# Performance work log

Measured on AMD Instinct MI355X. Metric: run time of the kernel, lower is better.

The kernel has to match this reference:

```python
import jax, jax.numpy as jnp
from jax import lax
import numpy as np

B, T, D, K = 64, 512, 768, 32


def setup_inputs() -> dict:
    key = jax.random.key(0)
    ks = jax.random.split(key, 6)
    x = jax.random.normal(ks[0], (B, T, D), dtype=jnp.float32)
    labels = jax.random.randint(ks[1], (B, T), 0, K)
    mask = jnp.ones((B, T), dtype=bool)  # mask[:,0] must be True for torchcrf
    W = jax.random.normal(ks[2], (D, K), dtype=jnp.float32) * (1.0 / np.sqrt(D))
    b = jnp.zeros((K,), dtype=jnp.float32)
    # CRF params (torchcrf init: uniform(-0.1, 0.1))
    start_trans = jax.random.uniform(ks[3], (K,), minval=-0.1, maxval=0.1, dtype=jnp.float32)
    end_trans = jax.random.uniform(ks[4], (K,), minval=-0.1, maxval=0.1, dtype=jnp.float32)
    trans = jax.random.uniform(ks[5], (K, K), minval=-0.1, maxval=0.1, dtype=jnp.float32)
    return {"x": x, "labels": labels, "mask": mask, "W": W, "b": b,
            "start_trans": start_trans, "end_trans": end_trans, "trans": trans}


def reference(x, labels, mask, W, b, start_trans, end_trans, trans):
    emissions = jnp.einsum('btd,dk->btk', x, W) + b  # [B,T,K]
    Bn, Tn, Kn = emissions.shape
    maskf = mask.astype(emissions.dtype)

    # ---- numerator: score of the gold tag path ----
    first_tags = labels[:, 0]
    num = start_trans[first_tags] + emissions[jnp.arange(Bn), 0, first_tags]
    prev, cur = labels[:, :-1], labels[:, 1:]
    em_gold = jnp.take_along_axis(emissions[:, 1:], cur[..., None], axis=-1)[..., 0]  # [B,T-1]
    num = num + jnp.sum((trans[prev, cur] + em_gold) * maskf[:, 1:], axis=1)
    seq_len = jnp.sum(mask.astype(jnp.int32), axis=1)  # [B]
    last_tags = jnp.take_along_axis(labels, (seq_len - 1)[:, None], axis=1)[:, 0]
    num = num + end_trans[last_tags]

    # ---- denominator: forward-algorithm log partition via scan ----
    def step(score, inp):
        em_t, m_t = inp  # em_t: [B,K], m_t: [B] bool
        # score[b,i] + trans[i,j] + em_t[b,j] -> logsumexp over i
        nxt = jax.nn.logsumexp(score[:, :, None] + trans[None, :, :] + em_t[:, None, :], axis=1)
        return jnp.where(m_t[:, None], nxt, score), None

    init = start_trans[None, :] + emissions[:, 0]  # [B,K]
    em_rest = jnp.swapaxes(emissions[:, 1:], 0, 1)  # [T-1,B,K]
    m_rest = jnp.swapaxes(mask[:, 1:], 0, 1)        # [T-1,B]
    score, _ = lax.scan(step, init, (em_rest, m_rest))
    denom = jax.nn.logsumexp(score + end_trans[None, :], axis=-1)  # [B]

    llh = num - denom
    return -jnp.mean(llh)  # module returns -crf(..., reduction='mean')
```

## Files before the change

### kernel.cpp

```cpp
#include <hip/hip_runtime.h>


#define BB 64
#define TT 512
#define DD 768
#define KK 32
#define INV_LN2 1.44269504088896f
#define LN2f    0.69314718055994f

typedef __attribute__((ext_vector_type(8))) short bf16x8;
typedef __attribute__((ext_vector_type(8))) _Float16 f16x8;
typedef __attribute__((ext_vector_type(4))) float f32x4;
typedef __attribute__((ext_vector_type(16))) float f32x16;

__device__ __forceinline__ float fexp2(float x) { float r; asm("v_exp_f32 %0, %1" : "=v"(r) : "v"(x)); return r; }
__device__ __forceinline__ float flog2(float x) { float r; asm("v_log_f32 %0, %1" : "=v"(r) : "v"(x)); return r; }

__device__ __forceinline__ bf16x8 cvt8(float4 a, float4 b) {
    union { int i[4]; bf16x8 v; } u;
    asm("v_cvt_pk_bf16_f32 %0, %1, %2" : "=v"(u.i[0]) : "v"(a.x), "v"(a.y));
    asm("v_cvt_pk_bf16_f32 %0, %1, %2" : "=v"(u.i[1]) : "v"(a.z), "v"(a.w));
    asm("v_cvt_pk_bf16_f32 %0, %1, %2" : "=v"(u.i[2]) : "v"(b.x), "v"(b.y));
    asm("v_cvt_pk_bf16_f32 %0, %1, %2" : "=v"(u.i[3]) : "v"(b.z), "v"(b.w));
    return u.v;
}
__device__ __forceinline__ bf16x8 asbf(float4 b) {
    union { float4 f; bf16x8 v; } u; u.f = b; return u.v;
}
__device__ __forceinline__ f16x8 frag4h(int a, int b, int c, int d) {
    union { int i[4]; f16x8 v; } u; u.i[0] = a; u.i[1] = b; u.i[2] = c; u.i[3] = d; return u.v;
}
__device__ __forceinline__ void plswap(int& a, int& b) {
    asm("v_permlane32_swap_b32 %0, %1" : "+v"(a), "+v"(b));
}
__device__ __forceinline__ int pkmulh(int a, int b) {
    int r; asm("v_pk_mul_f16 %0, %1, %2" : "=v"(r) : "v"(a), "v"(b)); return r;
}
__device__ __forceinline__ int cvtrep(float e) {
    int r; asm("v_cvt_pkrtz_f16_f32 %0, %1, %1" : "=v"(r) : "v"(e)); return r;
}
__device__ __forceinline__ int cvtpkh(float a, float b) {
    int r; asm("v_cvt_pkrtz_f16_f32 %0, %1, %2" : "=v"(r) : "v"(a), "v"(b)); return r;
}

__global__ __launch_bounds__(256) void pack_w(const float* __restrict__ W, float4* __restrict__ Wb)
{
    int idx = blockIdx.x * 256 + threadIdx.x;
    int l = idx & 63, slice = idx >> 6;
    int ks = slice >> 1, t = slice & 1;
    int c = (l & 15) + t * 16, g = l >> 4;
    int kr = ks * 32 + g * 8;
    float f0 = W[(kr + 0) * KK + c], f1 = W[(kr + 1) * KK + c];
    float f2 = W[(kr + 2) * KK + c], f3 = W[(kr + 3) * KK + c];
    float f4 = W[(kr + 4) * KK + c], f5 = W[(kr + 5) * KK + c];
    float f6 = W[(kr + 6) * KK + c], f7 = W[(kr + 7) * KK + c];
    union { int i[4]; float4 f; } u;
    asm("v_cvt_pk_bf16_f32 %0, %1, %2" : "=v"(u.i[0]) : "v"(f0), "v"(f1));
    asm("v_cvt_pk_bf16_f32 %0, %1, %2" : "=v"(u.i[1]) : "v"(f2), "v"(f3));
    asm("v_cvt_pk_bf16_f32 %0, %1, %2" : "=v"(u.i[2]) : "v"(f4), "v"(f5));
    asm("v_cvt_pk_bf16_f32 %0, %1, %2" : "=v"(u.i[3]) : "v"(f6), "v"(f7));
    Wb[idx] = u.f;
}

__global__ __launch_bounds__(256) void emis_kernel(
    const float* __restrict__ x, const float4* __restrict__ Wb,
    const float* __restrict__ bias, float* __restrict__ emlin)
{
    const int tid = threadIdx.x;
    const int l = tid & 63, wave = tid >> 6;
    const int r = l & 15, g = l >> 4;
    const int row0 = (blockIdx.x * 4 + wave) * 16;

    const float4* xA = (const float4*)x + (size_t)(row0 + r) * 192 + g * 2;
    const float4* wb = Wb + l;

    f32x4 acc0 = {0.f, 0.f, 0.f, 0.f};
    f32x4 acc1 = {0.f, 0.f, 0.f, 0.f};

    float4 s0a0, s0a1, s0b0, s0b1;
    float4 s1a0, s1a1, s1b0, s1b1;
    float4 s2a0, s2a1, s2b0, s2b1;
    float4 s3a0, s3a1, s3b0, s3b1;

#define LOADS(P, ks_) \
    P##a0 = xA[(ks_) * 8]; P##a1 = xA[(ks_) * 8 + 1]; \
    P##b0 = wb[(ks_) * 128]; P##b1 = wb[(ks_) * 128 + 64];
#define CONS(P) { \
    bf16x8 av = cvt8(P##a0, P##a1); \
    acc0 = __builtin_amdgcn_mfma_f32_16x16x32_bf16(av, asbf(P##b0), acc0, 0, 0, 0); \
    acc1 = __builtin_amdgcn_mfma_f32_16x16x32_bf16(av, asbf(P##b1), acc1, 0, 0, 0); }

    LOADS(s0, 0) LOADS(s1, 1) LOADS(s2, 2) LOADS(s3, 3)
    for (int ks = 0; ks < 20; ks += 4) {
        CONS(s0) LOADS(s0, ks + 4)
        CONS(s1) LOADS(s1, ks + 5)
        CONS(s2) LOADS(s2, ks + 6)
        CONS(s3) LOADS(s3, ks + 7)
    }
    CONS(s0) CONS(s1) CONS(s2) CONS(s3)
#undef LOADS
#undef CONS

    const int c0 = l & 15;
    const float b0 = bias[c0], b1 = bias[c0 + 16];
    #pragma unroll
    for (int reg = 0; reg < 4; ++reg) {
        const int orow = row0 + g * 4 + reg;
        emlin[(size_t)orow * KK + c0]      = fexp2((acc0[reg] + b0) * INV_LN2);
        emlin[(size_t)orow * KK + c0 + 16] = fexp2((acc1[reg] + b1) * INV_LN2);
    }
}

__global__ __launch_bounds__(64) void chain_kernel(
    const float* __restrict__ emlin, const float* __restrict__ trans,
    float* __restrict__ Qg, int* __restrict__ eag)
{
    __shared__ float els[34 * KK];

    const int g = blockIdx.x;
    const int b = g >> 4, u = g & 15;
    const int l = threadIdx.x;
    const int r32 = l & 31, hf = l >> 5;
    const float* el_g = emlin + (size_t)b * TT * KK;
    const int t0 = 32 * u + 1;

    #pragma unroll
    for (int i = 0; i < 17; ++i) {
        int idx = i * 64 + l;
        int gidx = t0 * KK + idx;
        if (gidx > TT * KK - 1) gidx = TT * KK - 1;
        els[idx] = el_g[gidx];
    }

    int M1p0, M1p1, M1p2, M1p3, M2p0, M2p1, M2p2, M2p3;
    {
        float m[16];
        #pragma unroll
        for (int e = 0; e < 8; ++e) {
            m[e]     = fexp2(trans[(hf * 8 + e) * KK + r32] * INV_LN2);
            m[e + 8] = fexp2(trans[(16 + hf * 8 + e) * KK + r32] * INV_LN2);
        }
        M1p0 = cvtpkh(m[0], m[1]);   M1p1 = cvtpkh(m[2], m[3]);
        M1p2 = cvtpkh(m[4], m[5]);   M1p3 = cvtpkh(m[6], m[7]);
        M2p0 = cvtpkh(m[8], m[9]);   M2p1 = cvtpkh(m[10], m[11]);
        M2p2 = cvtpkh(m[12], m[13]); M2p3 = cvtpkh(m[14], m[15]);
    }
    __syncthreads();

    int Ba0, Ba1, Ba2, Ba3, Ba4, Ba5, Ba6, Ba7;
    int Bb0, Bb1, Bb2, Bb3, Bb4, Bb5, Bb6, Bb7;
    {
        #define IDP(kl) (((r32 == (kl)) ? 0x3C00 : 0) | ((r32 == (kl) + 1) ? 0x3C000000 : 0))
        int k0 = hf * 8;
        Ba0 = IDP(k0);      Ba1 = IDP(k0 + 2);  Ba2 = IDP(k0 + 4);  Ba3 = IDP(k0 + 6);
        Ba4 = IDP(k0 + 16); Ba5 = IDP(k0 + 18); Ba6 = IDP(k0 + 20); Ba7 = IDP(k0 + 22);
        Bb0 = Ba0; Bb1 = Ba1; Bb2 = Ba2; Bb3 = Ba3;
        Bb4 = Ba4; Bb5 = Ba5; Bb6 = Ba6; Bb7 = Ba7;
        #undef IDP
    }
    const f32x16 zf = {0,0,0,0, 0,0,0,0, 0,0,0,0, 0,0,0,0};
    f32x16 acca = zf, accb = zf;
    int EEa = 0, EEb = 0;
    int eaca_ = 0, eacb_ = 0;

    float eva = els[r32];
    float evb = els[16 * KK + r32];

#define CLAMP14(E) ((E) < -14 ? -14 : ((E) > 14 ? 14 : (E)))

#define STEP1(X, rnext) { \
    int Ec = CLAMP14(EE##X); \
    eac##X##_ += Ec; \
    int scb = (15 - Ec) << 10; scb |= (scb << 16); \
    int ep = pkmulh(cvtrep(ev##X), scb); \
    ev##X = els[(rnext) * KK + r32]; \
    int A0 = pkmulh(M1p0, ep), A1 = pkmulh(M1p1, ep), A2 = pkmulh(M1p2, ep), A3 = pkmulh(M1p3, ep); \
    int A4 = pkmulh(M2p0, ep), A5 = pkmulh(M2p1, ep), A6 = pkmulh(M2p2, ep), A7 = pkmulh(M2p3, ep); \
    acc##X = __builtin_amdgcn_mfma_f32_32x32x16_f16(frag4h(A0, A1, A2, A3), \
                 frag4h(B##X##0, B##X##1, B##X##2, B##X##3), zf, 0, 0, 0); \
    acc##X = __builtin_amdgcn_mfma_f32_32x32x16_f16(frag4h(A4, A5, A6, A7), \
                 frag4h(B##X##4, B##X##5, B##X##6, B##X##7), acc##X, 0, 0, 0); \
    EE##X = (int)((((unsigned)__builtin_amdgcn_readfirstlane(__float_as_int(acc##X[0]))) >> 23) & 0xFFu) - 127; \
    int u0 = cvtpkh(acc##X[0],  acc##X[1]),  u1 = cvtpkh(acc##X[2],  acc##X[3]); \
    int u2 = cvtpkh(acc##X[4],  acc##X[5]),  u3 = cvtpkh(acc##X[6],  acc##X[7]); \
    int u4 = cvtpkh(acc##X[8],  acc##X[9]),  u5 = cvtpkh(acc##X[10], acc##X[11]); \
    int u6 = cvtpkh(acc##X[12], acc##X[13]), u7 = cvtpkh(acc##X[14], acc##X[15]); \
    plswap(u0, u2); plswap(u1, u3); plswap(u4, u6); plswap(u5, u7); \
    B##X##0 = u0; B##X##1 = u1; B##X##2 = u2; B##X##3 = u3; \
    B##X##4 = u4; B##X##5 = u5; B##X##6 = u6; B##X##7 = u7; \
}

#define STEP2(rna, rnb) { \
    int EcA = CLAMP14(EEa), EcB = CLAMP14(EEb); \
    eaca_ += EcA; eacb_ += EcB; \
    int scbA = (15 - EcA) << 10; scbA |= (scbA << 16); \
    int scbB = (15 - EcB) << 10; scbB |= (scbB << 16); \
    int epA = pkmulh(cvtrep(eva), scbA); \
    int epB = pkmulh(cvtrep(evb), scbB); \
    eva = els[(rna) * KK + r32]; \
    evb = els[(rnb) * KK + r32]; \
    int Aa0 = pkmulh(M1p0, epA), Aa1 = pkmulh(M1p1, epA), Aa2 = pkmulh(M1p2, epA), Aa3 = pkmulh(M1p3, epA); \
    int Ab0 = pkmulh(M1p0, epB), Ab1 = pkmulh(M1p1, epB), Ab2 = pkmulh(M1p2, epB), Ab3 = pkmulh(M1p3, epB); \
    int Aa4 = pkmulh(M2p0, epA), Aa5 = pkmulh(M2p1, epA), Aa6 = pkmulh(M2p2, epA), Aa7 = pkmulh(M2p3, epA); \
    int Ab4 = pkmulh(M2p0, epB), Ab5 = pkmulh(M2p1, epB), Ab6 = pkmulh(M2p2, epB), Ab7 = pkmulh(M2p3, epB); \
    acca = __builtin_amdgcn_mfma_f32_32x32x16_f16(frag4h(Aa0, Aa1, Aa2, Aa3), \
               frag4h(Ba0, Ba1, Ba2, Ba3), zf, 0, 0, 0); \
    accb = __builtin_amdgcn_mfma_f32_32x32x16_f16(frag4h(Ab0, Ab1, Ab2, Ab3), \
               frag4h(Bb0, Bb1, Bb2, Bb3), zf, 0, 0, 0); \
    acca = __builtin_amdgcn_mfma_f32_32x32x16_f16(frag4h(Aa4, Aa5, Aa6, Aa7), \
               frag4h(Ba4, Ba5, Ba6, Ba7), acca, 0, 0, 0); \
    accb = __builtin_amdgcn_mfma_f32_32x32x16_f16(frag4h(Ab4, Ab5, Ab6, Ab7), \
               frag4h(Bb4, Bb5, Bb6, Bb7), accb, 0, 0, 0); \
    EEa = (int)((((unsigned)__builtin_amdgcn_readfirstlane(__float_as_int(acca[0]))) >> 23) & 0xFFu) - 127; \
    int ua0 = cvtpkh(acca[0],  acca[1]),  ua1 = cvtpkh(acca[2],  acca[3]); \
    int ua2 = cvtpkh(acca[4],  acca[5]),  ua3 = cvtpkh(acca[6],  acca[7]); \
    int ua4 = cvtpkh(acca[8],  acca[9]),  ua5 = cvtpkh(acca[10], acca[11]); \
    int ua6 = cvtpkh(acca[12], acca[13]), ua7 = cvtpkh(acca[14], acca[15]); \
    EEb = (int)((((unsigned)__builtin_amdgcn_readfirstlane(__float_as_int(accb[0]))) >> 23) & 0xFFu) - 127; \
    int ub0 = cvtpkh(accb[0],  accb[1]),  ub1 = cvtpkh(accb[2],  accb[3]); \
    int ub2 = cvtpkh(accb[4],  accb[5]),  ub3 = cvtpkh(accb[6],  accb[7]); \
    int ub4 = cvtpkh(accb[8],  accb[9]),  ub5 = cvtpkh(accb[10], accb[11]); \
    int ub6 = cvtpkh(accb[12], accb[13]), ub7 = cvtpkh(accb[14], accb[15]); \
    plswap(ua0, ua2); plswap(ua1, ua3); plswap(ua4, ua6); plswap(ua5, ua7); \
    plswap(ub0, ub2); plswap(ub1, ub3); plswap(ub4, ub6); plswap(ub5, ub7); \
    Ba0 = ua0; Ba1 = ua1; Ba2 = ua2; Ba3 = ua3; \
    Ba4 = ua4; Ba5 = ua5; Ba6 = ua6; Ba7 = ua7; \
    Bb0 = ub0; Bb1 = ub1; Bb2 = ub2; Bb3 = ub3; \
    Bb4 = ub4; Bb5 = ub5; Bb6 = ub6; Bb7 = ub7; \
}

    #pragma unroll 1
    for (int s = 0; s < 15; ++s) {
        STEP2(s + 1, 17 + s)
    }
    if (u < 15) { STEP2(16, 32) }
    else        { STEP1(a, 16) }
#undef STEP1
#undef STEP2
#undef CLAMP14

    float* Qa = Qg + (size_t)(b * 32 + 2 * u) * 1024;
    float* Qb = Qa + 1024;
    #pragma unroll
    for (int i = 0; i < 16; ++i) {
        int row = (i & 3) + 8 * (i >> 2) + 4 * hf;
        Qa[row * KK + r32] = acca[i];
        Qb[row * KK + r32] = accb[i];
    }
    if (l == 0) { eag[b * 32 + 2 * u] = eaca_; eag[b * 32 + 2 * u + 1] = eacb_; }
}

__global__ __launch_bounds__(64) void combine_kernel(
    const float* __restrict__ emlin, const int* __restrict__ labels,
    const float* __restrict__ start, const float* __restrict__ endt,
    const float* __restrict__ trans, const float* __restrict__ Qg,
    const int* __restrict__ eag, float* __restrict__ llh)
{
    __shared__ float trs[KK * KK];
    __shared__ float wlds[KK];

    const int b = blockIdx.x, l = threadIdx.x;
    const int r32 = l & 31, hf = l >> 5;
    const float* el_g = emlin + (size_t)b * TT * KK;

    for (int i = 0; i < 16; ++i) trs[i * 64 + l] = trans[i * 64 + l];
    __syncthreads();

    const int* lab = labels + b * TT;
    float num = 0.f;
    #pragma unroll
    for (int c = 0; c < 8; ++c) {
        int t = c * 64 + l;
        int cur = lab[t];
        float v = LN2f * flog2(el_g[t * KK + cur]);
        v += (t == 0) ? start[cur] : trs[lab[t - 1] * KK + cur];
        if (t == TT - 1) v += endt[cur];
        num += v;
    }
    #pragma unroll
    for (int o = 32; o; o >>= 1) num += __shfl_xor(num, o);

    if (l < KK) wlds[l] = fexp2(start[l] * INV_LN2) * el_g[l];
    __syncthreads();

    const float4* Qbase = (const float4*)(Qg + (size_t)b * 32 * 1024);
    const int qoff = r32 * 8 + hf * 4;
    const int* eab = eag + b * 32;

    float4 qa0 = Qbase[qoff], qa1 = Qbase[qoff + 1], qa2 = Qbase[qoff + 2], qa3 = Qbase[qoff + 3];
    int Etot = 0;
    float sres = 0.f;
    for (int c = 0; c < 32; ++c) {
        int cn = (c + 1) & 31;
        float4 qb0 = Qbase[cn * 256 + qoff],     qb1 = Qbase[cn * 256 + qoff + 1];
        float4 qb2 = Qbase[cn * 256 + qoff + 2], qb3 = Qbase[cn * 256 + qoff + 3];
        const float4* wv = (const float4*)wlds + hf * 4;
        float4 w0 = wv[0], w1 = wv[1], w2 = wv[2], w3 = wv[3];
        float s = qa0.x * w0.x + qa0.y * w0.y + qa0.z * w0.z + qa0.w * w0.w
                + qa1.x * w1.x + qa1.y * w1.y + qa1.z * w1.z + qa1.w * w1.w
                + qa2.x * w2.x + qa2.y * w2.y + qa2.z * w2.z + qa2.w * w2.w
                + qa3.x * w3.x + qa3.y * w3.y + qa3.z * w3.z + qa3.w * w3.w;
        s += __shfl_xor(s, 32);
        int e0 = (int)((((unsigned)__builtin_amdgcn_readfirstlane(__float_as_int(s))) >> 23) & 0xFFu) - 127;
        if (e0 < -126) e0 = -126;
        if (e0 > 126) e0 = 126;
        Etot += eab[c] + e0;
        sres = s * __int_as_float((127 - e0) << 23);
        __syncthreads();
        if (l < KK) wlds[l] = sres;
        __syncthreads();
        qa0 = qb0; qa1 = qb1; qa2 = qb2; qa3 = qb3;
    }

    float tv = sres * fexp2(endt[r32] * INV_LN2);
    #pragma unroll
    for (int o = 16; o; o >>= 1) tv += __shfl_xor(tv, o);
    float denom = LN2f * ((float)Etot + flog2(tv));
    if (l == 0) llh[b] = num - denom;
}

__global__ __launch_bounds__(64) void reduce_kernel(
    const float* __restrict__ llh, float* __restrict__ out)
{
    const int l = threadIdx.x;
    float v = llh[l];
    #pragma unroll
    for (int o = 32; o; o >>= 1) v += __shfl_xor(v, o);
    if (l == 0) out[0] = -v * (1.0f / BB);
}

extern "C" void kernel_launch(void* const* d_in, const int* in_sizes, int n_in,
                              void* d_out, int out_size, void* d_ws, size_t ws_size,
                              hipStream_t stream)
{
    const float* x      = (const float*)d_in[0];
    const int*   labels = (const int*)  d_in[1];
    const float* W      = (const float*)d_in[3];
    const float* bias   = (const float*)d_in[4];
    const float* start  = (const float*)d_in[5];
    const float* endt   = (const float*)d_in[6];
    const float* trans  = (const float*)d_in[7];
    float* out  = (float*)d_out;

    char* ws = (char*)d_ws;
    float*  emlin = (float*)ws;
    float4* Wb    = (float4*)(ws + (4u << 20));
    float*  Qg    = (float*)(ws + (4u << 20) + (64u << 10));
    int*    eag   = (int*)(ws + (12u << 20) + (64u << 10));
    float*  llh   = (float*)(ws + (12u << 20) + (128u << 10));

    pack_w<<<dim3(12), dim3(256), 0, stream>>>(W, Wb);
    emis_kernel<<<dim3(512), dim3(256), 0, stream>>>(x, Wb, bias, emlin);
    chain_kernel<<<dim3(1024), dim3(64), 0, stream>>>(emlin, trans, Qg, eag);
    combine_kernel<<<dim3(BB), dim3(64), 0, stream>>>(emlin, labels, start, endt, trans, Qg, eag, llh);
    reduce_kernel<<<dim3(1), dim3(64), 0, stream>>>(llh, out);
}
```

Before: 54.87 us.

## Fold weight packing into emission kernel and reduction into combine via atomics

Removes the separate pack_w launch: each emission block now converts W to bf16 into a 48KB shared-memory tile and reads its B operands from LDS. Removes the final reduce launch: combine blocks add fixed-point quantized llh values into a 64-bit atomic, and the last block to finish writes the mean. This cuts two kernel launches and their dependencies, at the cost of every emission block redundantly converting W (extra global reads and a barrier), heavier LDS use per block, and fixed-point rounding in the final sum.

```diff
diff --git a/kernel.cpp b/kernel.cpp
--- a/kernel.cpp
+++ b/kernel.cpp
@@ -43,36 +43,39 @@
     int r; asm("v_cvt_pkrtz_f16_f32 %0, %1, %2" : "=v"(r) : "v"(a), "v"(b)); return r;
 }
 
-__global__ __launch_bounds__(256) void pack_w(const float* __restrict__ W, float4* __restrict__ Wb)
-{
-    int idx = blockIdx.x * 256 + threadIdx.x;
-    int l = idx & 63, slice = idx >> 6;
-    int ks = slice >> 1, t = slice & 1;
-    int c = (l & 15) + t * 16, g = l >> 4;
-    int kr = ks * 32 + g * 8;
-    float f0 = W[(kr + 0) * KK + c], f1 = W[(kr + 1) * KK + c];
-    float f2 = W[(kr + 2) * KK + c], f3 = W[(kr + 3) * KK + c];
-    float f4 = W[(kr + 4) * KK + c], f5 = W[(kr + 5) * KK + c];
-    float f6 = W[(kr + 6) * KK + c], f7 = W[(kr + 7) * KK + c];
-    union { int i[4]; float4 f; } u;
-    asm("v_cvt_pk_bf16_f32 %0, %1, %2" : "=v"(u.i[0]) : "v"(f0), "v"(f1));
-    asm("v_cvt_pk_bf16_f32 %0, %1, %2" : "=v"(u.i[1]) : "v"(f2), "v"(f3));
-    asm("v_cvt_pk_bf16_f32 %0, %1, %2" : "=v"(u.i[2]) : "v"(f4), "v"(f5));
-    asm("v_cvt_pk_bf16_f32 %0, %1, %2" : "=v"(u.i[3]) : "v"(f6), "v"(f7));
-    Wb[idx] = u.f;
-}
-
 __global__ __launch_bounds__(256) void emis_kernel(
-    const float* __restrict__ x, const float4* __restrict__ Wb,
+    const float* __restrict__ x, const float* __restrict__ W,
     const float* __restrict__ bias, float* __restrict__ emlin)
 {
+    __shared__ float4 WbL[3072];
+
     const int tid = threadIdx.x;
+
+    #pragma unroll
+    for (int u0 = 0; u0 < 12; ++u0) {
+        int idx = u0 * 256 + tid;
+        int ll = idx & 63, slice = idx >> 6;
+        int ks = slice >> 1, tt = slice & 1;
+        int c = (ll & 15) + tt * 16, gg = ll >> 4;
+        int kr = ks * 32 + gg * 8;
+        float f0 = W[(kr + 0) * KK + c], f1 = W[(kr + 1) * KK + c];
+        float f2 = W[(kr + 2) * KK + c], f3 = W[(kr + 3) * KK + c];
+        float f4 = W[(kr + 4) * KK + c], f5 = W[(kr + 5) * KK + c];
+        float f6 = W[(kr + 6) * KK + c], f7 = W[(kr + 7) * KK + c];
+        union { int i[4]; float4 f; } u;
+        asm("v_cvt_pk_bf16_f32 %0, %1, %2" : "=v"(u.i[0]) : "v"(f0), "v"(f1));
+        asm("v_cvt_pk_bf16_f32 %0, %1, %2" : "=v"(u.i[1]) : "v"(f2), "v"(f3));
+        asm("v_cvt_pk_bf16_f32 %0, %1, %2" : "=v"(u.i[2]) : "v"(f4), "v"(f5));
+        asm("v_cvt_pk_bf16_f32 %0, %1, %2" : "=v"(u.i[3]) : "v"(f6), "v"(f7));
+        WbL[idx] = u.f;
+    }
+    __syncthreads();
+
     const int l = tid & 63, wave = tid >> 6;
     const int r = l & 15, g = l >> 4;
     const int row0 = (blockIdx.x * 4 + wave) * 16;
 
     const float4* xA = (const float4*)x + (size_t)(row0 + r) * 192 + g * 2;
-    const float4* wb = Wb + l;
 
     f32x4 acc0 = {0.f, 0.f, 0.f, 0.f};
     f32x4 acc1 = {0.f, 0.f, 0.f, 0.f};
@@ -84,7 +87,7 @@
 
 #define LOADS(P, ks_) \
     P##a0 = xA[(ks_) * 8]; P##a1 = xA[(ks_) * 8 + 1]; \
-    P##b0 = wb[(ks_) * 128]; P##b1 = wb[(ks_) * 128 + 64];
+    P##b0 = WbL[(ks_) * 128 + l]; P##b1 = WbL[(ks_) * 128 + 64 + l];
 #define CONS(P) { \
     bf16x8 av = cvt8(P##a0, P##a1); \
     acc0 = __builtin_amdgcn_mfma_f32_16x16x32_bf16(av, asbf(P##b0), acc0, 0, 0, 0); \
@@ -113,7 +116,8 @@
 
 __global__ __launch_bounds__(64) void chain_kernel(
     const float* __restrict__ emlin, const float* __restrict__ trans,
-    float* __restrict__ Qg, int* __restrict__ eag)
+    float* __restrict__ Qg, int* __restrict__ eag,
+    unsigned long long* __restrict__ gsum, unsigned* __restrict__ gcnt)
 {
     __shared__ float els[34 * KK];
 
@@ -123,6 +127,8 @@
     const int r32 = l & 31, hf = l >> 5;
     const float* el_g = emlin + (size_t)b * TT * KK;
     const int t0 = 32 * u + 1;
+
+    if (g == 0 && l == 0) { atomicExch(gsum, 0ull); atomicExch(gcnt, 0u); }
 
     #pragma unroll
     for (int i = 0; i < 17; ++i) {
@@ -254,7 +260,8 @@
     const float* __restrict__ emlin, const int* __restrict__ labels,
     const float* __restrict__ start, const float* __restrict__ endt,
     const float* __restrict__ trans, const float* __restrict__ Qg,
-    const int* __restrict__ eag, float* __restrict__ llh)
+    const int* __restrict__ eag, unsigned long long* __restrict__ gsum,
+    unsigned* __restrict__ gcnt, float* __restrict__ out)
 {
     __shared__ float trs[KK * KK];
     __shared__ float wlds[KK];
@@ -316,17 +323,18 @@
     #pragma unroll
     for (int o = 16; o; o >>= 1) tv += __shfl_xor(tv, o);
     float denom = LN2f * ((float)Etot + flog2(tv));
-    if (l == 0) llh[b] = num - denom;
-}
-
-__global__ __launch_bounds__(64) void reduce_kernel(
-    const float* __restrict__ llh, float* __restrict__ out)
-{
-    const int l = threadIdx.x;
-    float v = llh[l];
-    #pragma unroll
-    for (int o = 32; o; o >>= 1) v += __shfl_xor(v, o);
-    if (l == 0) out[0] = -v * (1.0f / BB);
+    if (l == 0) {
+        float llh = num - denom;
+        long long q = llrintf(llh * 1048576.0f);
+        atomicAdd(gsum, (unsigned long long)q);
+        __threadfence();
+        unsigned done = atomicAdd(gcnt, 1u);
+        if (done == BB - 1) {
+            unsigned long long sfull = atomicAdd(gsum, 0ull);
+            long long ss = (long long)sfull;
+            out[0] = -(float)((double)ss * (1.0 / (1048576.0 * (double)BB)));
+        }
+    }
 }
 
 extern "C" void kernel_launch(void* const* d_in, const int* in_sizes, int n_in,
@@ -344,14 +352,12 @@
 
     char* ws = (char*)d_ws;
     float*  emlin = (float*)ws;
-    float4* Wb    = (float4*)(ws + (4u << 20));
-    float*  Qg    = (float*)(ws + (4u << 20) + (64u << 10));
-    int*    eag   = (int*)(ws + (12u << 20) + (64u << 10));
-    float*  llh   = (float*)(ws + (12u << 20) + (128u << 10));
-
-    pack_w<<<dim3(12), dim3(256), 0, stream>>>(W, Wb);
-    emis_kernel<<<dim3(512), dim3(256), 0, stream>>>(x, Wb, bias, emlin);
-    chain_kernel<<<dim3(1024), dim3(64), 0, stream>>>(emlin, trans, Qg, eag);
-    combine_kernel<<<dim3(BB), dim3(64), 0, stream>>>(emlin, labels, start, endt, trans, Qg, eag, llh);
-    reduce_kernel<<<dim3(1), dim3(64), 0, stream>>>(llh, out);
-}
+    float*  Qg    = (float*)(ws + (4u << 20));
+    int*    eag   = (int*)(ws + (12u << 20));
+    unsigned long long* gsum = (unsigned long long*)(ws + (12u << 20) + (16u << 10));
+    unsigned*           gcnt = (unsigned*)(ws + (12u << 20) + (16u << 10) + 8);
+
+    emis_kernel<<<dim3(512), dim3(256), 0, stream>>>(x, W, bias, emlin);
+    chain_kernel<<<dim3(1024), dim3(64), 0, stream>>>(emlin, trans, Qg, eag, gsum, gcnt);
+    combine_kernel<<<dim3(BB), dim3(64), 0, stream>>>(emlin, labels, start, endt, trans, Qg, eag, gsum, gcnt, out);
+}
```

Measured after the change: 50.62 us. 7.7% less time.
